# Performance work log

Hardware: AMD Instinct MI355X
Metric: run time of the kernel (lower is better)

The kernel has to match this reference:

```python
import jax, jax.numpy as jnp
import numpy as np


def setup_inputs() -> dict:
    key = jax.random.key(0)
    ks = jax.random.split(key, 5)
    B, H, W, C, R = 4, 64, 64, 256, 32
    x = jax.random.normal(ks[0], (B, H, W, C), dtype=jnp.float32)
    # 1x1 conv kernels stored as [C_in, C_out] matrices (equivalent math)
    w_f = jax.random.normal(ks[1], (C, R), dtype=jnp.float32) * (1.0 / np.sqrt(C))
    w_g = jax.random.normal(ks[2], (C, R), dtype=jnp.float32) * (1.0 / np.sqrt(C))
    w_h = jax.random.normal(ks[3], (C, R), dtype=jnp.float32) * (1.0 / np.sqrt(C))
    w_v = jax.random.normal(ks[4], (R, C), dtype=jnp.float32) * (1.0 / np.sqrt(R))
    gamma = jnp.zeros((1,), dtype=jnp.float32)
    return {"x": x, "w_f": w_f, "w_g": w_g, "w_h": w_h, "w_v": w_v, "gamma": gamma}


def reference(x, w_f, w_g, w_h, w_v, gamma):
    B, H, W, C = x.shape
    N = H * W
    xt = x.reshape(B, N, C)                       # flatten spatial tokens
    f = jnp.einsum('bnc,cr->bnr', xt, w_f)        # 1x1 conv == token-wise matmul
    g = jnp.einsum('bnc,cr->bnr', xt, w_g)
    h = jnp.einsum('bnc,cr->bnr', xt, w_h)
    scores = jnp.einsum('bnr,bmr->bnm', f, g)     # [B, N, N]
    # NOTE: original softmaxes over axis=1 (the query/row axis), not axis=-1
    attn = jax.nn.softmax(scores, axis=1)
    y = jnp.einsum('bnm,bmr->bnr', attn, h)       # [B, N, R]
    y = jnp.einsum('bnr,rc->bnc', y, w_v)         # output 1x1 conv
    y = y.reshape(B, H, W, C)
    return gamma * y + x
```

## Files before the change

kernel.cpp:

```cpp
#include <hip/hip_runtime.h>


#define BB 4
#define NN 4096
#define CC 256
#define RR 32
#define CSEG 4
#define LOG2E 1.44269504088896340736f

typedef short short8 __attribute__((ext_vector_type(8)));
typedef short short4v __attribute__((ext_vector_type(4)));
typedef unsigned short ushort8 __attribute__((ext_vector_type(8)));
typedef float floatx4 __attribute__((ext_vector_type(4)));

#define MFMA16 __builtin_amdgcn_mfma_f32_16x16x32_bf16
#define MFMA16K __builtin_amdgcn_mfma_f32_16x16x16bf16_1k

static __device__ __forceinline__ unsigned short f2bf(float f) {
  union { float f; unsigned u; } v; v.f = f;
  const unsigned r = v.u + 0x7fffu + ((v.u >> 16) & 1u);
  return (unsigned short)(r >> 16);
}
static __device__ __forceinline__ unsigned bfpack(float lo, float hi) {
  return __builtin_amdgcn_perm(__float_as_uint(hi), __float_as_uint(lo), 0x07060302u);
}

__global__ __launch_bounds__(256) void k_fgh(
    const float* __restrict__ x, const float* __restrict__ wf,
    const float* __restrict__ wg, const float* __restrict__ wh,
    const float* __restrict__ wv, unsigned short* __restrict__ f16,
    unsigned short* __restrict__ g16, unsigned short* __restrict__ hT16,
    unsigned short* __restrict__ wvfrag) {
  __shared__ unsigned short wflds[24576];
  const int tid = threadIdx.x, lane = tid & 63, wave = tid >> 6;
  const int col = lane & 15, q = lane >> 4;
  {
    const float* mats[3] = {wf, wg, wh};
#pragma unroll
    for (int mat = 0; mat < 3; ++mat) {
      const float* w = mats[mat];
#pragma unroll
      for (int rnd = 0; rnd < 8; ++rnd) {
        const int e = rnd * 1024 + tid * 4;
        const float4 v = *(const float4*)(w + e);
        const int k = e >> 5;
        const int n0 = e & 31;
        const int base = mat * 8192 + (((k >> 3) & 3) * 16) * 8 + (k & 7) +
                         (k >> 5) * 1024;
        const float vv[4] = {v.x, v.y, v.z, v.w};
#pragma unroll
        for (int t = 0; t < 4; ++t) {
          const int n = n0 + t;
          wflds[base + (n >> 4) * 512 + (n & 15) * 8] = f2bf(vv[t]);
        }
      }
    }
    if (blockIdx.x < 32) {
      const int idx = blockIdx.x * 256 + tid;
      const int t = (idx >> 9) & 15;
      const int l2 = (idx >> 3) & 63;
      const int c2 = l2 & 15, q2 = l2 >> 4;
      const int j = idx & 7;
      wvfrag[idx] = f2bf(wv[(q2 * 8 + j) * CC + t * 16 + c2]);
    }
  }
  const int t0 = blockIdx.x * 64 + wave * 16;
  short8 af[8];
  const float* xr = x + (long)(t0 + col) * CC + q * 8;
#pragma unroll
  for (int kc = 0; kc < 8; ++kc) {
    float tmp[8];
    *(float4*)(tmp) = *(const float4*)(xr + kc * 32);
    *(float4*)(tmp + 4) = *(const float4*)(xr + kc * 32 + 4);
    short8 o;
#pragma unroll
    for (int j = 0; j < 8; ++j) o[j] = (short)f2bf(tmp[j]);
    af[kc] = o;
  }
  __syncthreads();
  const floatx4 zero = {0.f, 0.f, 0.f, 0.f};
  floatx4 acc[3][2];
#pragma unroll
  for (int m = 0; m < 3; ++m) { acc[m][0] = zero; acc[m][1] = zero; }
#pragma unroll
  for (int kc = 0; kc < 8; ++kc) {
#pragma unroll
    for (int mat = 0; mat < 3; ++mat) {
#pragma unroll
      for (int nt = 0; nt < 2; ++nt) {
        const short8 bf = *(const short8*)(wflds + (mat * 16 + kc * 2 + nt) * 512 + lane * 8);
        acc[mat][nt] = MFMA16(af[kc], bf, acc[mat][nt], 0, 0, 0);
      }
    }
  }
  const int b = t0 >> 12;
#pragma unroll
  for (int nt = 0; nt < 2; ++nt) {
#pragma unroll
    for (int r = 0; r < 4; ++r) {
      const int tok = t0 + q * 4 + r;
      const int n = nt * 16 + col;
      f16[(long)tok * RR + n] = f2bf(acc[0][nt][r] * LOG2E);
      g16[(long)tok * RR + n] = f2bf(acc[1][nt][r]);
      const int tl = tok & (NN - 1);
      const int sp = (tl & ~31) | (q << 3) | ((tl & 16) >> 2) | r;
      hT16[((long)b * RR + n) * NN + sp] = f2bf(acc[2][nt][r]);
    }
  }
}

__global__ __launch_bounds__(256) void k_colsum(
    const unsigned short* __restrict__ f16, const unsigned short* __restrict__ g16,
    float* __restrict__ psum) {
  __shared__ float red[4][32];
  const int tid = threadIdx.x, lane = tid & 63, wave = tid >> 6;
  const int col = lane & 15, q = lane >> 4;
  const int mblk = blockIdx.x & 127;
  const int b = (blockIdx.x >> 7) & 3;
  const int seg = blockIdx.x >> 9;
  const int m0 = mblk * 32;
  const short8 bg1 = *(const short8*)(g16 + ((long)(b * NN + m0 + col)) * RR + q * 8);
  const short8 bg2 = *(const short8*)(g16 + ((long)(b * NN + m0 + 16 + col)) * RR + q * 8);
  const floatx4 zero = {0.f, 0.f, 0.f, 0.f};
  float s1 = 0.f, s2 = 0.f;
  const unsigned short* fb =
      f16 + ((long)b * NN + seg * (NN / CSEG) + wave * (NN / CSEG / 4)) * RR;
#pragma unroll 4
  for (int n = 0; n < NN / CSEG / 4; n += 16) {
    const short8 af = *(const short8*)(fb + (long)(n + col) * RR + q * 8);
    const floatx4 d1 = MFMA16(af, bg1, zero, 0, 0, 0);
    const floatx4 d2 = MFMA16(af, bg2, zero, 0, 0, 0);
    s1 += __builtin_amdgcn_exp2f(d1[0]) + __builtin_amdgcn_exp2f(d1[1]) +
          __builtin_amdgcn_exp2f(d1[2]) + __builtin_amdgcn_exp2f(d1[3]);
    s2 += __builtin_amdgcn_exp2f(d2[0]) + __builtin_amdgcn_exp2f(d2[1]) +
          __builtin_amdgcn_exp2f(d2[2]) + __builtin_amdgcn_exp2f(d2[3]);
  }
  s1 += __shfl_xor(s1, 16); s1 += __shfl_xor(s1, 32);
  s2 += __shfl_xor(s2, 16); s2 += __shfl_xor(s2, 32);
  if (lane < 16) {
    red[wave][lane] = s1;
    red[wave][lane + 16] = s2;
  }
  __syncthreads();
  if (tid < 32) {
    psum[(long)seg * (BB * NN) + b * NN + m0 + tid] =
        red[0][tid] + red[1][tid] + red[2][tid] + red[3][tid];
  }
}

__global__ __launch_bounds__(512, 4) void k_pvout(
    const unsigned short* __restrict__ f16, const unsigned short* __restrict__ g16,
    const unsigned short* __restrict__ hT16, const float* __restrict__ psum,
    const unsigned short* __restrict__ wvfrag, const float* __restrict__ x,
    const float* __restrict__ gamma, float* __restrict__ out) {
  __shared__ float ylds[8][32 * 36];
  __shared__ float sc_all[8][16 * 36];
  __shared__ float bias[NN];
  const int tid = threadIdx.x, lane = tid & 63, wave = tid >> 6;
  const int col = lane & 15, q = lane >> 4;
  const int b = blockIdx.x >> 7;
  const int t0 = (blockIdx.x & 127) * 32;
  const floatx4 zero = {0.f, 0.f, 0.f, 0.f};
  {
    float cs[8] = {0.f, 0.f, 0.f, 0.f, 0.f, 0.f, 0.f, 0.f};
#pragma unroll
    for (int sg = 0; sg < CSEG; ++sg) {
      const float* p = psum + (long)sg * (BB * NN) + b * NN + tid * 8;
      const float4 a = *(const float4*)p;
      const float4 c = *(const float4*)(p + 4);
      cs[0] += a.x; cs[1] += a.y; cs[2] += a.z; cs[3] += a.w;
      cs[4] += c.x; cs[5] += c.y; cs[6] += c.z; cs[7] += c.w;
    }
#pragma unroll
    for (int j = 0; j < 8; ++j) bias[tid * 8 + j] = -__builtin_amdgcn_logf(cs[j]);
  }
  const short8 af1 = *(const short8*)(f16 + ((long)(b * NN + t0 + col)) * RR + q * 8);
  const short8 af2 = *(const short8*)(f16 + ((long)(b * NN + t0 + 16 + col)) * RR + q * 8);
  floatx4 a11 = zero, a12 = zero, a21 = zero, a22 = zero;
  const unsigned short* gb = g16 + (long)b * NN * RR;
  const unsigned short* hb = hT16 + (long)b * RR * NN;
  const int mq = wave * 512;
  __syncthreads();
#pragma unroll 2
  for (int mi = 0; mi < 512; mi += 32) {
    const int m0 = mq + mi;
    const short8 bg1 = *(const short8*)(gb + (long)(m0 + col) * RR + q * 8);
    const short8 bg2 = *(const short8*)(gb + (long)(m0 + 16 + col) * RR + q * 8);
    const short8 hv1 = *(const short8*)(hb + (long)col * NN + m0 + q * 8);
    const short8 hv2 = *(const short8*)(hb + (long)(col + 16) * NN + m0 + q * 8);
    const floatx4 cm0 = *(const floatx4*)(bias + m0 + q * 4);
    const floatx4 cm1 = *(const floatx4*)(bias + m0 + 16 + q * 4);
    const floatx4 d00 = MFMA16(bg1, af1, cm0, 0, 0, 0);
    const floatx4 d01 = MFMA16(bg2, af1, cm1, 0, 0, 0);
    const floatx4 d10 = MFMA16(bg1, af2, cm0, 0, 0, 0);
    const floatx4 d11 = MFMA16(bg2, af2, cm1, 0, 0, 0);
    union PU { unsigned u[2]; short4v s; } p00, p01, p10, p11;
    p00.u[0] = bfpack(__builtin_amdgcn_exp2f(d00[0]), __builtin_amdgcn_exp2f(d00[1]));
    p00.u[1] = bfpack(__builtin_amdgcn_exp2f(d00[2]), __builtin_amdgcn_exp2f(d00[3]));
    p01.u[0] = bfpack(__builtin_amdgcn_exp2f(d01[0]), __builtin_amdgcn_exp2f(d01[1]));
    p01.u[1] = bfpack(__builtin_amdgcn_exp2f(d01[2]), __builtin_amdgcn_exp2f(d01[3]));
    p10.u[0] = bfpack(__builtin_amdgcn_exp2f(d10[0]), __builtin_amdgcn_exp2f(d10[1]));
    p10.u[1] = bfpack(__builtin_amdgcn_exp2f(d10[2]), __builtin_amdgcn_exp2f(d10[3]));
    p11.u[0] = bfpack(__builtin_amdgcn_exp2f(d11[0]), __builtin_amdgcn_exp2f(d11[1]));
    p11.u[1] = bfpack(__builtin_amdgcn_exp2f(d11[2]), __builtin_amdgcn_exp2f(d11[3]));
    const short4v bh1lo = __builtin_shufflevector(hv1, hv1, 0, 1, 2, 3);
    const short4v bh1hi = __builtin_shufflevector(hv1, hv1, 4, 5, 6, 7);
    const short4v bh2lo = __builtin_shufflevector(hv2, hv2, 0, 1, 2, 3);
    const short4v bh2hi = __builtin_shufflevector(hv2, hv2, 4, 5, 6, 7);
    a11 = MFMA16K(p00.s, bh1lo, a11, 0, 0, 0);
    a11 = MFMA16K(p01.s, bh1hi, a11, 0, 0, 0);
    a12 = MFMA16K(p00.s, bh2lo, a12, 0, 0, 0);
    a12 = MFMA16K(p01.s, bh2hi, a12, 0, 0, 0);
    a21 = MFMA16K(p10.s, bh1lo, a21, 0, 0, 0);
    a21 = MFMA16K(p11.s, bh1hi, a21, 0, 0, 0);
    a22 = MFMA16K(p10.s, bh2lo, a22, 0, 0, 0);
    a22 = MFMA16K(p11.s, bh2hi, a22, 0, 0, 0);
  }
  {
    float* yp = &ylds[wave][0];
#pragma unroll
    for (int r = 0; r < 4; ++r) {
      yp[(q * 4 + r) * 36 + col] = a11[r];
      yp[(q * 4 + r) * 36 + col + 16] = a12[r];
      yp[(16 + q * 4 + r) * 36 + col] = a21[r];
      yp[(16 + q * 4 + r) * 36 + col + 16] = a22[r];
    }
  }
  __syncthreads();
  {
    const int tile = wave & 1, hh = wave >> 1;
    float s[8] = {0.f, 0.f, 0.f, 0.f, 0.f, 0.f, 0.f, 0.f};
#pragma unroll
    for (int w2 = 0; w2 < 8; ++w2) {
      const float* yp = &ylds[w2][(tile * 16 + col) * 36 + q * 8];
      const float4 u0 = *(const float4*)yp;
      const float4 u1 = *(const float4*)(yp + 4);
      s[0] += u0.x; s[1] += u0.y; s[2] += u0.z; s[3] += u0.w;
      s[4] += u1.x; s[5] += u1.y; s[6] += u1.z; s[7] += u1.w;
    }
    short8 ay;
#pragma unroll
    for (int j = 0; j < 8; ++j) ay[j] = (short)f2bf(s[j]);
    const float gm = gamma[0];
    float* sc = &sc_all[wave][0];
    const int row = lane >> 2, c4 = (lane & 3) * 4;
#pragma unroll
    for (int tp = 0; tp < 4; tp += 2) {
      const short8 bw0 = *(const short8*)(wvfrag + (hh * 4 + tp) * 512 + lane * 8);
      const short8 bw1 = *(const short8*)(wvfrag + (hh * 4 + tp + 1) * 512 + lane * 8);
      const floatx4 d0 = MFMA16(ay, bw0, zero, 0, 0, 0);
      const floatx4 d1 = MFMA16(ay, bw1, zero, 0, 0, 0);
#pragma unroll
      for (int r = 0; r < 4; ++r) {
        sc[(q * 4 + r) * 36 + col] = d0[r];
        sc[(q * 4 + r) * 36 + col + 16] = d1[r];
      }
#pragma unroll
      for (int j = 0; j < 2; ++j) {
        const float4 v = *(const float4*)(sc + row * 36 + c4 + j * 16);
        const long gidx = (long)(b * NN + t0 + tile * 16 + row) * CC +
                          hh * 64 + tp * 16 + j * 16 + c4;
        const float4 xv = *(const float4*)(x + gidx);
        float4 o;
        o.x = gm * v.x + xv.x; o.y = gm * v.y + xv.y;
        o.z = gm * v.z + xv.z; o.w = gm * v.w + xv.w;
        *(float4*)(out + gidx) = o;
      }
    }
  }
}

extern "C" void kernel_launch(void* const* d_in, const int* in_sizes, int n_in,
                              void* d_out, int out_size, void* d_ws, size_t ws_size,
                              hipStream_t stream) {
  const float* x = (const float*)d_in[0];
  const float* wf = (const float*)d_in[1];
  const float* wg = (const float*)d_in[2];
  const float* wh = (const float*)d_in[3];
  const float* wv = (const float*)d_in[4];
  const float* gamma = (const float*)d_in[5];
  float* out = (float*)d_out;

  unsigned short* f16 = (unsigned short*)d_ws;
  unsigned short* g16 = f16 + (long)BB * NN * RR;
  unsigned short* hT16 = g16 + (long)BB * NN * RR;
  unsigned short* wvfrag = hT16 + (long)BB * NN * RR;
  float* psum = (float*)(wvfrag + 8192);

  k_fgh<<<BB * NN / 64, 256, 0, stream>>>(x, wf, wg, wh, wv, f16, g16, hT16, wvfrag);
  k_colsum<<<CSEG * BB * 128, 256, 0, stream>>>(f16, g16, psum);
  k_pvout<<<BB * 128, 512, 0, stream>>>(f16, g16, hT16, psum, wvfrag, x, gamma, out);
}
```

Baseline: 120.5 us.

## Split k_fgh reduction dimension across two wave groups with LDS reduction

Doubles the k_fgh block to 512 threads, so each group of four waves computes half of the C=256 reduction for the same 64 tokens. The partial accumulators are combined through a new LDS buffer before the stores. The x loads are also moved ahead of the weight staging so their global latency overlaps with the LDS weight fill. The cost is a second barrier, extra LDS traffic, and half the waves sitting idle during the output stage.

```diff
diff --git a/kernel.cpp b/kernel.cpp
--- a/kernel.cpp
+++ b/kernel.cpp
@@ -25,23 +25,38 @@
   return __builtin_amdgcn_perm(__float_as_uint(hi), __float_as_uint(lo), 0x07060302u);
 }
 
-__global__ __launch_bounds__(256) void k_fgh(
+__global__ __launch_bounds__(512) void k_fgh(
     const float* __restrict__ x, const float* __restrict__ wf,
     const float* __restrict__ wg, const float* __restrict__ wh,
     const float* __restrict__ wv, unsigned short* __restrict__ f16,
     unsigned short* __restrict__ g16, unsigned short* __restrict__ hT16,
     unsigned short* __restrict__ wvfrag) {
   __shared__ unsigned short wflds[24576];
+  __shared__ float accred[4][64][25];
   const int tid = threadIdx.x, lane = tid & 63, wave = tid >> 6;
   const int col = lane & 15, q = lane >> 4;
+  const int tg = wave & 3, kh = wave >> 2;
+  const int t0 = blockIdx.x * 64 + tg * 16;
+  short8 af[4];
+  const float* xr = x + (long)(t0 + col) * CC + kh * 128 + q * 8;
+#pragma unroll
+  for (int kc = 0; kc < 4; ++kc) {
+    float tmp[8];
+    *(float4*)(tmp) = *(const float4*)(xr + kc * 32);
+    *(float4*)(tmp + 4) = *(const float4*)(xr + kc * 32 + 4);
+    short8 o;
+#pragma unroll
+    for (int j = 0; j < 8; ++j) o[j] = (short)f2bf(tmp[j]);
+    af[kc] = o;
+  }
   {
     const float* mats[3] = {wf, wg, wh};
 #pragma unroll
     for (int mat = 0; mat < 3; ++mat) {
       const float* w = mats[mat];
 #pragma unroll
-      for (int rnd = 0; rnd < 8; ++rnd) {
-        const int e = rnd * 1024 + tid * 4;
+      for (int rnd = 0; rnd < 4; ++rnd) {
+        const int e = rnd * 2048 + tid * 4;
         const float4 v = *(const float4*)(w + e);
         const int k = e >> 5;
         const int n0 = e & 31;
@@ -55,8 +70,8 @@
         }
       }
     }
-    if (blockIdx.x < 32) {
-      const int idx = blockIdx.x * 256 + tid;
+    if (blockIdx.x < 16) {
+      const int idx = blockIdx.x * 512 + tid;
       const int t = (idx >> 9) & 15;
       const int l2 = (idx >> 3) & 63;
       const int c2 = l2 & 15, q2 = l2 >> 4;
@@ -64,47 +79,60 @@
       wvfrag[idx] = f2bf(wv[(q2 * 8 + j) * CC + t * 16 + c2]);
     }
   }
-  const int t0 = blockIdx.x * 64 + wave * 16;
-  short8 af[8];
-  const float* xr = x + (long)(t0 + col) * CC + q * 8;
-#pragma unroll
-  for (int kc = 0; kc < 8; ++kc) {
-    float tmp[8];
-    *(float4*)(tmp) = *(const float4*)(xr + kc * 32);
-    *(float4*)(tmp + 4) = *(const float4*)(xr + kc * 32 + 4);
-    short8 o;
-#pragma unroll
-    for (int j = 0; j < 8; ++j) o[j] = (short)f2bf(tmp[j]);
-    af[kc] = o;
-  }
   __syncthreads();
   const floatx4 zero = {0.f, 0.f, 0.f, 0.f};
   floatx4 acc[3][2];
 #pragma unroll
   for (int m = 0; m < 3; ++m) { acc[m][0] = zero; acc[m][1] = zero; }
 #pragma unroll
-  for (int kc = 0; kc < 8; ++kc) {
+  for (int kc = 0; kc < 4; ++kc) {
+    const int kc2 = kh * 4 + kc;
 #pragma unroll
     for (int mat = 0; mat < 3; ++mat) {
 #pragma unroll
       for (int nt = 0; nt < 2; ++nt) {
-        const short8 bf = *(const short8*)(wflds + (mat * 16 + kc * 2 + nt) * 512 + lane * 8);
+        const short8 bf = *(const short8*)(wflds + (mat * 16 + kc2 * 2 + nt) * 512 + lane * 8);
         acc[mat][nt] = MFMA16(af[kc], bf, acc[mat][nt], 0, 0, 0);
       }
     }
   }
-  const int b = t0 >> 12;
-#pragma unroll
-  for (int nt = 0; nt < 2; ++nt) {
-#pragma unroll
-    for (int r = 0; r < 4; ++r) {
-      const int tok = t0 + q * 4 + r;
-      const int n = nt * 16 + col;
-      f16[(long)tok * RR + n] = f2bf(acc[0][nt][r] * LOG2E);
-      g16[(long)tok * RR + n] = f2bf(acc[1][nt][r]);
-      const int tl = tok & (NN - 1);
-      const int sp = (tl & ~31) | (q << 3) | ((tl & 16) >> 2) | r;
-      hT16[((long)b * RR + n) * NN + sp] = f2bf(acc[2][nt][r]);
+  if (kh == 1) {
+#pragma unroll
+    for (int mat = 0; mat < 3; ++mat) {
+#pragma unroll
+      for (int nt = 0; nt < 2; ++nt) {
+#pragma unroll
+        for (int r = 0; r < 4; ++r) {
+          accred[tg][lane][(mat * 2 + nt) * 4 + r] = acc[mat][nt][r];
+        }
+      }
+    }
+  }
+  __syncthreads();
+  if (kh == 0) {
+#pragma unroll
+    for (int mat = 0; mat < 3; ++mat) {
+#pragma unroll
+      for (int nt = 0; nt < 2; ++nt) {
+#pragma unroll
+        for (int r = 0; r < 4; ++r) {
+          acc[mat][nt][r] += accred[tg][lane][(mat * 2 + nt) * 4 + r];
+        }
+      }
+    }
+    const int b = t0 >> 12;
+#pragma unroll
+    for (int nt = 0; nt < 2; ++nt) {
+#pragma unroll
+      for (int r = 0; r < 4; ++r) {
+        const int tok = t0 + q * 4 + r;
+        const int n = nt * 16 + col;
+        f16[(long)tok * RR + n] = f2bf(acc[0][nt][r] * LOG2E);
+        g16[(long)tok * RR + n] = f2bf(acc[1][nt][r]);
+        const int tl = tok & (NN - 1);
+        const int sp = (tl & ~31) | (q << 3) | ((tl & 16) >> 2) | r;
+        hT16[((long)b * RR + n) * NN + sp] = f2bf(acc[2][nt][r]);
+      }
     }
   }
 }
@@ -287,7 +315,7 @@
   unsigned short* wvfrag = hT16 + (long)BB * NN * RR;
   float* psum = (float*)(wvfrag + 8192);
 
-  k_fgh<<<BB * NN / 64, 256, 0, stream>>>(x, wf, wg, wh, wv, f16, g16, hT16, wvfrag);
+  k_fgh<<<BB * NN / 64, 512, 0, stream>>>(x, wf, wg, wh, wv, f16, g16, hT16, wvfrag);
   k_colsum<<<CSEG * BB * 128, 256, 0, stream>>>(f16, g16, psum);
   k_pvout<<<BB * 128, 512, 0, stream>>>(f16, g16, hT16, psum, wvfrag, x, gamma, out);
 }
```

Measured after the change: 120.5 us. About the same (+0.0%).
